# Kernel tuning notes

Measured on AMD Instinct MI355X. Metric: run time of the kernel, lower is better.

The kernel has to match this reference:

```python
import jax, jax.numpy as jnp
import numpy as np


def setup_inputs() -> dict:
    key = jax.random.key(0)
    ks = jax.random.split(key, 7)
    B, T, D, H, A = 1024, 512, 32, 128, 10
    s = lambda *sh: 1.0 / np.sqrt(H)
    return {
        "x": jax.random.normal(ks[0], (B, T, D), dtype=jnp.float32),
        "W_ih": jax.random.normal(ks[1], (4 * H, D), dtype=jnp.float32) * (1.0 / np.sqrt(H)),
        "W_hh": jax.random.normal(ks[2], (4 * H, H), dtype=jnp.float32) * (1.0 / np.sqrt(H)),
        "b_ih": jax.random.normal(ks[3], (4 * H,), dtype=jnp.float32) * (1.0 / np.sqrt(H)),
        "b_hh": jax.random.normal(ks[4], (4 * H,), dtype=jnp.float32) * (1.0 / np.sqrt(H)),
        "fc_w": jax.random.normal(ks[5], (A, H), dtype=jnp.float32) * (1.0 / np.sqrt(H)),
        "fc_b": jax.random.normal(ks[6], (A,), dtype=jnp.float32) * (1.0 / np.sqrt(H)),
    }


def _lstm(x, W_ih, W_hh, b_ih, b_hh):
    # x: (B, T, D). PyTorch gate order: i, f, g, o packed along 4H rows.
    B, T, D = x.shape
    H = W_hh.shape[1]
    # Precompute input projections for all timesteps in one GEMM: (B,T,4H)
    x_proj = jnp.einsum('btd,gd->btg', x, W_ih) + b_ih + b_hh
    h0 = jnp.zeros((B, H), dtype=x.dtype)
    c0 = jnp.zeros((B, H), dtype=x.dtype)

    def step(carry, xp_t):
        h, c = carry
        gates = xp_t + h @ W_hh.T  # (B, 4H)
        i, f, g, o = jnp.split(gates, 4, axis=-1)
        i = jax.nn.sigmoid(i)
        f = jax.nn.sigmoid(f)
        g = jnp.tanh(g)
        o = jax.nn.sigmoid(o)
        c_new = f * c + i * g
        h_new = o * jnp.tanh(c_new)
        return (h_new, c_new), None

    (h_n, c_n), _ = jax.lax.scan(step, (h0, c0), jnp.swapaxes(x_proj, 0, 1))
    return h_n, c_n


def reference(x, W_ih, W_hh, b_ih, b_hh, fc_w, fc_b):
    h_n, c_n = _lstm(x, W_ih, W_hh, b_ih, b_hh)
    # out[:, -1, :] == h_n for a single-layer LSTM
    q_values = h_n @ fc_w.T + fc_b  # (B, A)
    return q_values, h_n[None], c_n[None]  # hidden states with num_layers=1 leading dim
```

## Files before the change

### kernel.cpp

```cpp
#include <hip/hip_runtime.h>

typedef short  short8  __attribute__((ext_vector_type(8)));
typedef float  floatx4 __attribute__((ext_vector_type(4)));

#define TT 512
#define DD 32
#define HH 128
#define AA 10
#define LOG2E 1.44269504088896340736f

__device__ __forceinline__ unsigned f2bf(float f) {
    unsigned u = __builtin_bit_cast(unsigned, f);
    return (u + 0x7fffu + ((u >> 16) & 1u)) >> 16;
}

__device__ __forceinline__ short8 cvt8(floatx4 a, floatx4 b) {
    short8 r;
    r[0] = (short)f2bf(a[0]); r[1] = (short)f2bf(a[1]);
    r[2] = (short)f2bf(a[2]); r[3] = (short)f2bf(a[3]);
    r[4] = (short)f2bf(b[0]); r[5] = (short)f2bf(b[1]);
    r[6] = (short)f2bf(b[2]); r[7] = (short)f2bf(b[3]);
    return r;
}

__device__ __forceinline__ float sig2(float a) {
    return __builtin_amdgcn_rcpf(1.0f + __builtin_amdgcn_exp2f(a));
}
__device__ __forceinline__ float tanh2(float a) {
    return 1.0f - 2.0f * __builtin_amdgcn_rcpf(1.0f + __builtin_amdgcn_exp2f(a));
}

__device__ __forceinline__ void step_barrier() {
    asm volatile("s_waitcnt lgkmcnt(0)" ::: "memory");
    __builtin_amdgcn_s_barrier();
    asm volatile("" ::: "memory");
}

__global__ __launch_bounds__(256)
void xcvt(const float* __restrict__ x, unsigned short* __restrict__ xb) {
    const long i = (long)blockIdx.x * 256 + threadIdx.x;
    floatx4 a = *(const floatx4*)(x + 8 * i);
    floatx4 b = *(const floatx4*)(x + 8 * i + 4);
    *(short8*)(xb + 8 * i) = cvt8(a, b);
}

template<int USEWS>
__global__ __launch_bounds__(512, 2)
void lstm_fused(const float* __restrict__ x,    const unsigned short* __restrict__ xbf,
                const float* __restrict__ W_ih, const float* __restrict__ W_hh,
                const float* __restrict__ b_ih, const float* __restrict__ b_hh,
                const float* __restrict__ fc_w, const float* __restrict__ fc_b,
                float* __restrict__ out)
{
    __shared__ unsigned short h_lds[2][4 * HH];
    __shared__ float hq[4][HH + 4];

    const int tid  = threadIdx.x;
    const int lane = tid & 63;
    const int w    = tid >> 6;
    const int l15  = lane & 15;
    const int lgrp = lane >> 4;
    const int bloc = l15 & 3;

    const long bglob = (long)blockIdx.x * 4 + bloc;

    short8  afr[4][5];
    floatx4 biasv[4];
    #pragma unroll
    for (int tg = 0; tg < 4; ++tg) {
        const float sc = (tg == 2) ? (2.0f * LOG2E) : (-LOG2E);
        const int m  = w + 8 * tg;
        const int ga = 16 * m + l15;
        #pragma unroll
        for (int s = 0; s < 4; ++s) {
            const float* p = W_hh + ga * HH + 32 * s + 8 * lgrp;
            afr[tg][s] = cvt8(*(const floatx4*)p * sc, *(const floatx4*)(p + 4) * sc);
        }
        {
            const float* p = W_ih + ga * DD + 8 * lgrp;
            afr[tg][4] = cvt8(*(const floatx4*)p * sc, *(const floatx4*)(p + 4) * sc);
        }
        #pragma unroll
        for (int r = 0; r < 4; ++r) {
            const int gd = 16 * m + 4 * lgrp + r;
            biasv[tg][r] = (b_ih[gd] + b_hh[gd]) * sc;
        }
    }
    const floatx4 zf = {0.f, 0.f, 0.f, 0.f};

    ((unsigned*)h_lds)[tid] = 0u;
    __syncthreads();

    short8  xf;
    floatx4 xa, xb_;
    if constexpr (USEWS) {
        xf = *(const short8*)(xbf + (bglob * TT) * DD + 8 * lgrp);
    } else {
        xa  = *(const floatx4*)(x + (bglob * TT) * DD + 8 * lgrp);
        xb_ = *(const floatx4*)(x + (bglob * TT) * DD + 8 * lgrp + 4);
    }

    const int rs  = l15 >> 2;
    const bool sb0 = (rs & 1) != 0;
    const bool sb1 = (rs & 2) != 0;
    const int bp  = bloc;
    const int jp  = 16 * w + 4 * lgrp + rs;
    float cval = 0.f, hval = 0.f;
    const int hwr_off = (bp * 256 + 2 * jp) ^ ((bp & 1) << 6);

    int cur = 0;
    for (int t = 0; t < TT; ++t) {
        short8 xcur;
        const int tn = (t + 1 < TT) ? (t + 1) : (TT - 1);
        if constexpr (USEWS) {
            xcur = xf;
            xf = *(const short8*)(xbf + (bglob * TT + tn) * DD + 8 * lgrp);
        } else {
            xcur = cvt8(xa, xb_);
            const float* xp = x + (bglob * TT + tn) * DD + 8 * lgrp;
            xa  = *(const floatx4*)(xp);
            xb_ = *(const floatx4*)(xp + 4);
        }

        short8 hb[4];
        const char* hbase = (const char*)h_lds[cur];
        #pragma unroll
        for (int s = 0; s < 4; ++s) {
            const int off = (bloc * 256 + 64 * s + 16 * lgrp) ^ ((bloc & 1) << 6);
            hb[s] = *(const short8*)(hbase + off);
        }

        floatx4 accA[4], accB[4];
        #pragma unroll
        for (int tg = 0; tg < 4; ++tg)
            accA[tg] = __builtin_amdgcn_mfma_f32_16x16x32_bf16(afr[tg][4], xcur, biasv[tg], 0, 0, 0);
        #pragma unroll
        for (int tg = 0; tg < 4; ++tg)
            accB[tg] = __builtin_amdgcn_mfma_f32_16x16x32_bf16(afr[tg][0], hb[0], zf, 0, 0, 0);
        #pragma unroll
        for (int tg = 0; tg < 4; ++tg)
            accA[tg] = __builtin_amdgcn_mfma_f32_16x16x32_bf16(afr[tg][1], hb[1], accA[tg], 0, 0, 0);
        #pragma unroll
        for (int tg = 0; tg < 4; ++tg)
            accB[tg] = __builtin_amdgcn_mfma_f32_16x16x32_bf16(afr[tg][2], hb[2], accB[tg], 0, 0, 0);
        #pragma unroll
        for (int tg = 0; tg < 4; ++tg)
            accA[tg] = __builtin_amdgcn_mfma_f32_16x16x32_bf16(afr[tg][3], hb[3], accA[tg], 0, 0, 0);

        float g4[4];
        #pragma unroll
        for (int tg = 0; tg < 4; ++tg) {
            floatx4 sv = accA[tg] + accB[tg];
            const float v01 = sb0 ? sv[1] : sv[0];
            const float v23 = sb0 ? sv[3] : sv[2];
            g4[tg] = sb1 ? v23 : v01;
        }

        const float iv = sig2(g4[0]);
        const float fv = sig2(g4[1]);
        const float gv = tanh2(g4[2]);
        const float ov = sig2(g4[3]);
        cval = fv * cval + iv * gv;
        hval = ov * tanh2(cval * (2.0f * LOG2E));

        *(unsigned short*)((char*)h_lds[cur ^ 1] + hwr_off) = (unsigned short)f2bf(hval);
        step_barrier();
        cur ^= 1;
    }

    {
        const long bg = (long)blockIdx.x * 4 + bp;
        out[10240 + bg * HH + jp]          = hval;
        out[10240 + 131072 + bg * HH + jp] = cval;
        hq[bp][jp] = hval;
    }
    __syncthreads();
    if (tid < 4 * AA) {
        const int b = tid / AA, a = tid - AA * b;
        float s = fc_b[a];
        const float* fw = fc_w + a * HH;
        const float* hr = &hq[b][0];
        #pragma unroll 8
        for (int j = 0; j < HH; ++j) s = fmaf(hr[j], fw[j], s);
        out[((long)blockIdx.x * 4 + b) * AA + a] = s;
    }
}

extern "C" void kernel_launch(void* const* d_in, const int* in_sizes, int n_in,
                              void* d_out, int out_size, void* d_ws, size_t ws_size,
                              hipStream_t stream) {
    const float* x    = (const float*)d_in[0];
    const float* W_ih = (const float*)d_in[1];
    const float* W_hh = (const float*)d_in[2];
    const float* b_ih = (const float*)d_in[3];
    const float* b_hh = (const float*)d_in[4];
    const float* fc_w = (const float*)d_in[5];
    const float* fc_b = (const float*)d_in[6];
    float* out = (float*)d_out;

    const size_t xelems = (size_t)1024 * TT * DD;
    if (ws_size >= xelems * sizeof(unsigned short)) {
        unsigned short* xb = (unsigned short*)d_ws;
        xcvt<<<dim3(8192), dim3(256), 0, stream>>>(x, xb);
        lstm_fused<1><<<dim3(256), dim3(512), 0, stream>>>(
            x, xb, W_ih, W_hh, b_ih, b_hh, fc_w, fc_b, out);
    } else {
        lstm_fused<0><<<dim3(256), dim3(512), 0, stream>>>(
            x, nullptr, W_ih, W_hh, b_ih, b_hh, fc_w, fc_b, out);
    }
}
```

Measured before the change: 323.2 us.

## Interleave two batch groups per block to overlap gate math with MFMAs

Each block now owns eight batch rows split into two groups of four. The recurrence is software-pipelined so that one group's sigmoid/tanh and h write-back run while the other group's recurrent MFMA chain runs, using four rotating LDS h buffers. A rotation-based LDS addressing replaces the XOR swizzle, and a packed bf16 convert instruction replaces the manual rounding. The launch still uses 256 blocks, so blocks 128-255 repeat the same work and suppress their writes. Per-block serial work and the number of barriers per timestep double.

New measurement: 537.1 us. 66.2% more time.

```diff
diff --git a/kernel.cpp b/kernel.cpp
--- a/kernel.cpp
+++ b/kernel.cpp
@@ -52,8 +52,8 @@
                 const float* __restrict__ fc_w, const float* __restrict__ fc_b,
                 float* __restrict__ out)
 {
-    __shared__ unsigned short h_lds[2][4 * HH];
-    __shared__ float hq[4][HH + 4];
+    __shared__ unsigned short h_lds[4][4 * HH];
+    __shared__ float hq[8][HH + 4];
 
     const int tid  = threadIdx.x;
     const int lane = tid & 63;
@@ -62,7 +62,9 @@
     const int lgrp = lane >> 4;
     const int bloc = l15 & 3;
 
-    const long bglob = (long)blockIdx.x * 4 + bloc;
+    const int  blk = blockIdx.x & 127;
+    const long bg0 = (long)blk * 8 + bloc;
+    const long bg1 = bg0 + 4;
 
     short8  afr[4][5];
     floatx4 biasv[4];
@@ -86,103 +88,130 @@
             biasv[tg][r] = (b_ih[gd] + b_hh[gd]) * sc;
         }
     }
-    const floatx4 zf = {0.f, 0.f, 0.f, 0.f};
-
-    ((unsigned*)h_lds)[tid] = 0u;
+
+    ((unsigned*)h_lds)[tid]       = 0u;
+    ((unsigned*)h_lds)[tid + 512] = 0u;
     __syncthreads();
-
-    short8  xf;
-    floatx4 xa, xb_;
-    if constexpr (USEWS) {
-        xf = *(const short8*)(xbf + (bglob * TT) * DD + 8 * lgrp);
-    } else {
-        xa  = *(const floatx4*)(x + (bglob * TT) * DD + 8 * lgrp);
-        xb_ = *(const floatx4*)(x + (bglob * TT) * DD + 8 * lgrp + 4);
-    }
 
     const int rs  = l15 >> 2;
     const bool sb0 = (rs & 1) != 0;
     const bool sb1 = (rs & 2) != 0;
     const int bp  = bloc;
     const int jp  = 16 * w + 4 * lgrp + rs;
-    float cval = 0.f, hval = 0.f;
-    const int hwr_off = (bp * 256 + 2 * jp) ^ ((bp & 1) << 6);
-
-    int cur = 0;
-    for (int t = 0; t < TT; ++t) {
-        short8 xcur;
-        const int tn = (t + 1 < TT) ? (t + 1) : (TT - 1);
+
+    const int rdR0 = bloc * 256 + ((  0 + 16 * lgrp + 32 * bloc) & 255);
+    const int rdR1 = bloc * 256 + (( 64 + 16 * lgrp + 32 * bloc) & 255);
+    const int rdR2 = bloc * 256 + ((128 + 16 * lgrp + 32 * bloc) & 255);
+    const int rdR3 = bloc * 256 + ((192 + 16 * lgrp + 32 * bloc) & 255);
+    const int wrR  = bp * 256 + ((2 * jp + 32 * bp) & 255);
+
+    short8  xf0, xf1;
+    floatx4 xa0, xb0, xa1, xb1;
+    if constexpr (USEWS) {
+        xf0 = *(const short8*)(xbf + (bg0 * TT) * DD + 8 * lgrp);
+        xf1 = *(const short8*)(xbf + (bg1 * TT) * DD + 8 * lgrp);
+    } else {
+        xa0 = *(const floatx4*)(x + (bg0 * TT) * DD + 8 * lgrp);
+        xb0 = *(const floatx4*)(x + (bg0 * TT) * DD + 8 * lgrp + 4);
+        xa1 = *(const floatx4*)(x + (bg1 * TT) * DD + 8 * lgrp);
+        xb1 = *(const floatx4*)(x + (bg1 * TT) * DD + 8 * lgrp + 4);
+    }
+
+    floatx4 acc0[4], acc1[4];
+    float cv0 = 0.f, hv0 = 0.f, cv1 = 0.f, hv1 = 0.f;
+    char* lb = (char*)h_lds;
+
+    auto PHASE = [&](floatx4 (&accC)[4], short8& xfC, floatx4& xaC, floatx4& xbC,
+                     const long bgC, int tC, int RDB,
+                     floatx4 (&accE)[4], float& cvE, float& hvE, int WRB,
+                     bool DOEW) {
+        short8 hb0 = *(const short8*)(lb + RDB + rdR0);
+        short8 hb1 = *(const short8*)(lb + RDB + rdR1);
+        short8 hb2 = *(const short8*)(lb + RDB + rdR2);
+        short8 hb3 = *(const short8*)(lb + RDB + rdR3);
+
+        short8 xc;
+        const int tn = (tC + 1 < TT) ? (tC + 1) : (TT - 1);
         if constexpr (USEWS) {
-            xcur = xf;
-            xf = *(const short8*)(xbf + (bglob * TT + tn) * DD + 8 * lgrp);
+            xc = xfC;
+            xfC = *(const short8*)(xbf + (bgC * TT + tn) * DD + 8 * lgrp);
         } else {
-            xcur = cvt8(xa, xb_);
-            const float* xp = x + (bglob * TT + tn) * DD + 8 * lgrp;
-            xa  = *(const floatx4*)(xp);
-            xb_ = *(const floatx4*)(xp + 4);
-        }
-
-        short8 hb[4];
-        const char* hbase = (const char*)h_lds[cur];
-        #pragma unroll
-        for (int s = 0; s < 4; ++s) {
-            const int off = (bloc * 256 + 64 * s + 16 * lgrp) ^ ((bloc & 1) << 6);
-            hb[s] = *(const short8*)(hbase + off);
-        }
-
-        floatx4 accA[4], accB[4];
-        #pragma unroll
-        for (int tg = 0; tg < 4; ++tg)
-            accA[tg] = __builtin_amdgcn_mfma_f32_16x16x32_bf16(afr[tg][4], xcur, biasv[tg], 0, 0, 0);
-        #pragma unroll
-        for (int tg = 0; tg < 4; ++tg)
-            accB[tg] = __builtin_amdgcn_mfma_f32_16x16x32_bf16(afr[tg][0], hb[0], zf, 0, 0, 0);
-        #pragma unroll
-        for (int tg = 0; tg < 4; ++tg)
-            accA[tg] = __builtin_amdgcn_mfma_f32_16x16x32_bf16(afr[tg][1], hb[1], accA[tg], 0, 0, 0);
-        #pragma unroll
-        for (int tg = 0; tg < 4; ++tg)
-            accB[tg] = __builtin_amdgcn_mfma_f32_16x16x32_bf16(afr[tg][2], hb[2], accB[tg], 0, 0, 0);
-        #pragma unroll
-        for (int tg = 0; tg < 4; ++tg)
-            accA[tg] = __builtin_amdgcn_mfma_f32_16x16x32_bf16(afr[tg][3], hb[3], accA[tg], 0, 0, 0);
-
-        float g4[4];
-        #pragma unroll
-        for (int tg = 0; tg < 4; ++tg) {
-            floatx4 sv = accA[tg] + accB[tg];
-            const float v01 = sb0 ? sv[1] : sv[0];
-            const float v23 = sb0 ? sv[3] : sv[2];
-            g4[tg] = sb1 ? v23 : v01;
-        }
-
-        const float iv = sig2(g4[0]);
-        const float fv = sig2(g4[1]);
-        const float gv = tanh2(g4[2]);
-        const float ov = sig2(g4[3]);
-        cval = fv * cval + iv * gv;
-        hval = ov * tanh2(cval * (2.0f * LOG2E));
-
-        *(unsigned short*)((char*)h_lds[cur ^ 1] + hwr_off) = (unsigned short)f2bf(hval);
+            xc = cvt8(xaC, xbC);
+            const float* xp = x + (bgC * TT + tn) * DD + 8 * lgrp;
+            xaC = *(const floatx4*)(xp);
+            xbC = *(const floatx4*)(xp + 4);
+        }
+
+        #pragma unroll
+        for (int tg = 0; tg < 4; ++tg)
+            accC[tg] = __builtin_amdgcn_mfma_f32_16x16x32_bf16(afr[tg][4], xc, biasv[tg], 0, 0, 0);
+
+        if (DOEW) {
+            float g4[4];
+            #pragma unroll
+            for (int tg = 0; tg < 4; ++tg) {
+                const float v01 = sb0 ? accE[tg][1] : accE[tg][0];
+                const float v23 = sb0 ? accE[tg][3] : accE[tg][2];
+                g4[tg] = sb1 ? v23 : v01;
+            }
+            const float iv = sig2(g4[0]);
+            const float fv = sig2(g4[1]);
+            const float gv = tanh2(g4[2]);
+            const float ov = sig2(g4[3]);
+            cvE = fv * cvE + iv * gv;
+            hvE = ov * tanh2(cvE * (2.0f * LOG2E));
+            unsigned hp;
+            asm("v_cvt_pk_bf16_f32 %0, %1, %2" : "=v"(hp) : "v"(hvE), "v"(hvE));
+            *(unsigned short*)(lb + WRB + wrR) = (unsigned short)hp;
+        }
+
+        __builtin_amdgcn_sched_barrier(0);
+
+        #pragma unroll
+        for (int tg = 0; tg < 4; ++tg)
+            accC[tg] = __builtin_amdgcn_mfma_f32_16x16x32_bf16(afr[tg][0], hb0, accC[tg], 0, 0, 0);
+        #pragma unroll
+        for (int tg = 0; tg < 4; ++tg)
+            accC[tg] = __builtin_amdgcn_mfma_f32_16x16x32_bf16(afr[tg][1], hb1, accC[tg], 0, 0, 0);
+        #pragma unroll
+        for (int tg = 0; tg < 4; ++tg)
+            accC[tg] = __builtin_amdgcn_mfma_f32_16x16x32_bf16(afr[tg][2], hb2, accC[tg], 0, 0, 0);
+        #pragma unroll
+        for (int tg = 0; tg < 4; ++tg)
+            accC[tg] = __builtin_amdgcn_mfma_f32_16x16x32_bf16(afr[tg][3], hb3, accC[tg], 0, 0, 0);
+
         step_barrier();
-        cur ^= 1;
-    }
-
-    {
-        const long bg = (long)blockIdx.x * 4 + bp;
-        out[10240 + bg * HH + jp]          = hval;
-        out[10240 + 131072 + bg * HH + jp] = cval;
-        hq[bp][jp] = hval;
-    }
+    };
+
+    PHASE(acc0, xf0, xa0, xb0, bg0, 0, 1 * 1024, acc1, cv1, hv1, 0, false);
+
+    #pragma unroll 1
+    for (int t = 0; t < TT; t += 2) {
+        PHASE(acc1, xf1, xa1, xb1, bg1, t,     3 * 1024, acc0, cv0, hv0, 0 * 1024, true);
+        PHASE(acc0, xf0, xa0, xb0, bg0, t + 1, 0 * 1024, acc1, cv1, hv1, 2 * 1024, true);
+        PHASE(acc1, xf1, xa1, xb1, bg1, t + 1, 2 * 1024, acc0, cv0, hv0, 1 * 1024, true);
+        PHASE(acc0, xf0, xa0, xb0, bg0, t + 2, 1 * 1024, acc1, cv1, hv1, 3 * 1024, true);
+    }
+
+    if (blockIdx.x < 128) {
+        const long b0 = (long)blk * 8 + bp;
+        const long b1 = b0 + 4;
+        out[10240 + b0 * HH + jp]          = hv0;
+        out[10240 + 131072 + b0 * HH + jp] = cv0;
+        out[10240 + b1 * HH + jp]          = hv1;
+        out[10240 + 131072 + b1 * HH + jp] = cv1;
+    }
+    hq[bp][jp]     = hv0;
+    hq[bp + 4][jp] = hv1;
     __syncthreads();
-    if (tid < 4 * AA) {
+    if (blockIdx.x < 128 && tid < 8 * AA) {
         const int b = tid / AA, a = tid - AA * b;
         float s = fc_b[a];
         const float* fw = fc_w + a * HH;
         const float* hr = &hq[b][0];
         #pragma unroll 8
         for (int j = 0; j < HH; ++j) s = fmaf(hr[j], fw[j], s);
-        out[((long)blockIdx.x * 4 + b) * AA + a] = s;
+        out[((long)blk * 8 + b) * AA + a] = s;
     }
 }
 
```
